# Performance work log

Hardware: AMD Instinct MI355X
Metric: run time of the kernel (lower is better)

## Reference

```python
import jax, jax.numpy as jnp
import numpy as np

STRIDE = 2

def setup_inputs() -> dict:
    key = jax.random.key(0)
    k1, k2, k3, k4, k5 = jax.random.split(key, 5)
    B, Cin, H, W = 16, 64, 128, 128
    Cout, kh, kw = 64, 3, 3
    oh = ow = 63  # ceil((H - kh + 1) / STRIDE)
    inp = jax.random.normal(k1, (B, Cin, H, W), dtype=jnp.float32)
    fan_in = Cin * kh * kw
    weight = jax.random.normal(k2, (Cout, Cin, kh, kw), dtype=jnp.float32) / np.sqrt(fan_in)
    bias = jax.random.normal(k3, (Cout,), dtype=jnp.float32) * 0.01
    selh = jax.random.randint(k4, (oh, ow), 0, STRIDE, dtype=jnp.int32)
    selw = jax.random.randint(k5, (oh, ow), 0, STRIDE, dtype=jnp.int32)
    return {"input": inp, "weight": weight, "bias": bias, "selh": selh, "selw": selw}


def reference(input, weight, bias, selh, selw):
    # Stochastic downsampled conv: per output pixel (i,j), pick the patch at
    # row i*stride + selh[i,j], col j*stride + selw[i,j], then apply the conv GEMM.
    Cout, Cin, kh, kw = weight.shape
    oh, ow = selh.shape
    # top-left corner of the selected patch for each output pixel
    rng_h = selh + jnp.arange(0, oh * STRIDE, STRIDE, dtype=jnp.int32)[:, None]   # (oh, ow)
    rng_w = selw + jnp.arange(0, ow * STRIDE, STRIDE, dtype=jnp.int32)[None, :]   # (oh, ow)
    # full patch index grids: (oh, ow, kh, kw)
    ih = rng_h[:, :, None, None] + jnp.arange(kh, dtype=jnp.int32)[None, None, :, None]
    iw = rng_w[:, :, None, None] + jnp.arange(kw, dtype=jnp.int32)[None, None, None, :]
    # gather selected im2col patches only (avoids materializing the full unfold)
    patches = input[:, :, ih, iw]  # (B, Cin, oh, ow, kh, kw)
    out = jnp.einsum('bcyxhw,ochw->boyx', patches, weight) + bias[None, :, None, None]
    return out  # (B, Cout, oh, ow)
```

## Files before the change

### kernel.cpp

```cpp
#include <hip/hip_runtime.h>


#define B_    16
#define CIN   64
#define H_    128
#define W_    128
#define COUT  64
#define OH    63
#define OW    63
#define NPIX  (OH * OW)
#define KTOT  (CIN * 9)

typedef short  short8  __attribute__((ext_vector_type(8)));
typedef float  float4v __attribute__((ext_vector_type(4)));

__device__ inline short f2bf(float f) {
    union { float f; unsigned u; } x; x.f = f;
    unsigned r = x.u + 0x7fffu + ((x.u >> 16) & 1u);
    return (short)(r >> 16);
}

__global__ __launch_bounds__(256)
void repack_bf16(const float* __restrict__ in, const float* __restrict__ wgt,
                 short* __restrict__ nhwc, short* __restrict__ wgt_t) {
    if (blockIdx.y == H_) {
        const int bid = blockIdx.z * 2 + blockIdx.x;
        for (int e = bid * 256 + (int)threadIdx.x; e < COUT * KTOT; e += 32 * 256) {
            const int o   = e / KTOT;
            const int rem = e - o * KTOT;
            const int c   = rem / 9;
            const int tap = rem - c * 9;
            wgt_t[o * KTOT + tap * CIN + c] = f2bf(wgt[e]);
        }
        return;
    }

    __shared__ float T[64 * 65];
    const int tid = threadIdx.x;
    const int w0  = blockIdx.x * 64;
    const int h   = blockIdx.y;
    const int b   = blockIdx.z;

    {
        const int w4 = tid & 15;
        const int cl = tid >> 4;
#pragma unroll
        for (int i = 0; i < 4; ++i) {
            const int c = cl + 16 * i;
            const float4 v = *(const float4*)&in[((b * CIN + c) * H_ + h) * W_ + w0 + 4 * w4];
            T[c * 65 + 4 * w4 + 0] = v.x;
            T[c * 65 + 4 * w4 + 1] = v.y;
            T[c * 65 + 4 * w4 + 2] = v.z;
            T[c * 65 + 4 * w4 + 3] = v.w;
        }
    }
    __syncthreads();
    {
        const int cg = tid & 7;
        const int wl = tid >> 3;
#pragma unroll
        for (int i = 0; i < 2; ++i) {
            const int w = wl + 32 * i;
            short8 v;
#pragma unroll
            for (int t = 0; t < 8; ++t)
                v[t] = f2bf(T[(8 * cg + t) * 65 + w]);
            *(short8*)&nhwc[((b * H_ + h) * W_ + w0 + w) * CIN + 8 * cg] = v;
        }
    }
}

#define PIXT  16
#define BT    2
#define LDO   65

__global__ __launch_bounds__(256, 4)
void sconv2davg_mfma(const short* __restrict__ nhwc,
                     const short* __restrict__ wgt_t,
                     const float* __restrict__ bias,
                     const int* __restrict__ selh,
                     const int* __restrict__ selw,
                     float* __restrict__ out) {
    __shared__ __align__(16) short As[18 * 1024];

    const int tid = threadIdx.x;
    const int p0  = blockIdx.x * PIXT;
    const int b0  = blockIdx.y * BT;

    const int ln = tid & 15;
    const int hl = (tid >> 4) & 3;
    const int wv = tid >> 6;
    const int l  = tid & 63;

    const short* Bp = &wgt_t[(16 * wv + ln) * KTOT + hl * 8];
    short8 Bv[18];
#pragma unroll
    for (int u = 0; u < 18; ++u) {
        const int cc = u / 9, tap = u - 9 * (u / 9);
        Bv[u] = *(const short8*)&Bp[tap * CIN + cc * 32];
    }

    {
        const int w01 = wv & 1;
        const int wcc = wv >> 1;
        const int mst = 16 * w01 + (l >> 2);
        const int pl  = mst >> 1;
        const int bl  = mst & 1;
        int p = p0 + pl;
        if (p > NPIX - 1) p = NPIX - 1;
        const int y   = p / OW;
        const int x   = p - y * OW;
        const int ih0 = 2 * y + selh[p];
        const int iw0 = 2 * x + selw[p];
        const short* src0 =
            &nhwc[(((b0 + bl) * H_ + ih0) * W_ + iw0) * CIN + wcc * 32 + (l & 3) * 8];
        short* dst0 = &As[wcc * 9 * 1024 + w01 * 512] + l * 8;
#pragma unroll
        for (int tap = 0; tap < 9; ++tap) {
            const int kh = tap / 3, kw = tap - 3 * (tap / 3);
            __builtin_amdgcn_global_load_lds(
                (const __attribute__((address_space(1))) void*)
                    (src0 + kh * (W_ * CIN) + kw * CIN),
                (__attribute__((address_space(3))) void*)(dst0 + tap * 1024),
                16, 0, 0);
        }
    }
    __syncthreads();

    float4v acc[2];
#pragma unroll
    for (int i = 0; i < 2; ++i) acc[i] = (float4v){0.f, 0.f, 0.f, 0.f};
#pragma unroll
    for (int u = 0; u < 18; ++u) {
#pragma unroll
        for (int i = 0; i < 2; ++i) {
            const short8 a = *(const short8*)
                &As[u * 1024 + (16 * i + ln) * 32 + hl * 8];
            acc[i] = __builtin_amdgcn_mfma_f32_16x16x32_bf16(a, Bv[u], acc[i], 0, 0, 0);
        }
    }
    __syncthreads();

    float* Ot = (float*)As;
    const float bv = bias[16 * wv + ln];
#pragma unroll
    for (int i = 0; i < 2; ++i)
#pragma unroll
        for (int r = 0; r < 4; ++r)
            Ot[(16 * i + 4 * hl + r) * LDO + 16 * wv + ln] = acc[i][r] + bv;
    __syncthreads();
    {
        const int pp = tid & 15;
        const int rr = tid >> 4;
        const int p2 = p0 + pp;
        if (p2 < NPIX) {
#pragma unroll
            for (int k = 0; k < 8; ++k) {
                const int rid = k * 16 + rr;
                const int b2  = rid >> 6;
                const int o   = rid & 63;
                out[((b0 + b2) * COUT + o) * NPIX + p2] = Ot[(pp * 2 + b2) * LDO + o];
            }
        }
    }
}

#define FKC   72
#define FLDA  76
__global__ __launch_bounds__(256, 4)
void sconv2davg_fallback(const float* __restrict__ in,
                         const float* __restrict__ wgt,
                         const float* __restrict__ bias,
                         const int* __restrict__ selh,
                         const int* __restrict__ selw,
                         float* __restrict__ out) {
    __shared__ float As[64 * FLDA];
    __shared__ float Ws[64 * FLDA];
    __shared__ int hb_s[4], wb_s[4];
    const int tid = threadIdx.x;
    const int p0  = blockIdx.x * 4;
    if (tid < 4) {
        int p = p0 + tid;
        if (p > NPIX - 1) p = NPIX - 1;
        int y = p / OW;
        int x = p - y * OW;
        hb_s[tid] = 2 * y + selh[p];
        wb_s[tid] = 2 * x + selw[p];
    }
    __syncthreads();
    const int tn = tid & 15, tm = tid >> 4;
    float acc[4][4];
#pragma unroll
    for (int i = 0; i < 4; ++i)
#pragma unroll
        for (int j = 0; j < 4; ++j) acc[i][j] = 0.0f;
    for (int cc = 0; cc < 8; ++cc) {
        const int c0 = cc * 8;
#pragma unroll
        for (int it = 0; it < 18; ++it) {
            int idx = tid + it * 256;
            int m = idx / FKC, rem = idx - m * FKC;
            int cl = rem / 9, r = rem - cl * 9;
            int kh = r / 3, kw = r - kh * 3;
            As[m * FLDA + rem] =
                in[((((m & 15) * CIN) + (c0 + cl)) * H_ + hb_s[m >> 4] + kh) * W_ + wb_s[m >> 4] + kw];
        }
#pragma unroll
        for (int it = 0; it < 18; ++it) {
            int idx = tid + it * 256;
            int o = idx / FKC, kk = idx - o * FKC;
            Ws[o * FLDA + kk] = wgt[o * KTOT + cc * FKC + kk];
        }
        __syncthreads();
#pragma unroll 2
        for (int k0 = 0; k0 < FKC; k0 += 4) {
            float4 a[4], w[4];
#pragma unroll
            for (int i = 0; i < 4; ++i) a[i] = *(const float4*)&As[(4 * tm + i) * FLDA + k0];
#pragma unroll
            for (int j = 0; j < 4; ++j) w[j] = *(const float4*)&Ws[(tn + 16 * j) * FLDA + k0];
#pragma unroll
            for (int i = 0; i < 4; ++i)
#pragma unroll
                for (int j = 0; j < 4; ++j) {
                    acc[i][j] += a[i].x * w[j].x; acc[i][j] += a[i].y * w[j].y;
                    acc[i][j] += a[i].z * w[j].z; acc[i][j] += a[i].w * w[j].w;
                }
        }
        __syncthreads();
    }
    const int p = p0 + (tm >> 2);
    if (p < NPIX) {
#pragma unroll
        for (int i = 0; i < 4; ++i) {
            int b = (tm & 3) * 4 + i;
#pragma unroll
            for (int j = 0; j < 4; ++j)
                out[((b * COUT) + tn + 16 * j) * NPIX + p] = acc[i][j] + bias[tn + 16 * j];
        }
    }
}

extern "C" void kernel_launch(void* const* d_in, const int* in_sizes, int n_in,
                              void* d_out, int out_size, void* d_ws, size_t ws_size,
                              hipStream_t stream) {
    const float* in   = (const float*)d_in[0];
    const float* wgt  = (const float*)d_in[1];
    const float* bias = (const float*)d_in[2];
    const int*   selh = (const int*)d_in[3];
    const int*   selw = (const int*)d_in[4];
    float* out = (float*)d_out;

    const size_t nhwc_elems = (size_t)B_ * H_ * W_ * CIN;
    const size_t need = (nhwc_elems + (size_t)COUT * KTOT) * 2;

    if (ws_size >= need) {
        short* nhwc  = (short*)d_ws;
        short* wgt_t = nhwc + nhwc_elems;
        repack_bf16<<<dim3(W_ / 64, H_ + 1, B_), 256, 0, stream>>>(in, wgt, nhwc, wgt_t);
        const int ptiles = (NPIX + PIXT - 1) / PIXT;
        sconv2davg_mfma<<<dim3(ptiles, B_ / BT), 256, 0, stream>>>(
            nhwc, wgt_t, bias, selh, selw, out);
    } else {
        sconv2davg_fallback<<<(NPIX + 3) / 4, 256, 0, stream>>>(
            in, wgt, bias, selh, selw, out);
    }
}
```

Measured before the change: 129.7 us.

## Process four pixel tiles per block with double-buffered LDS gather prefetch

Each MFMA conv block now handles four consecutive 16-pixel tiles instead of one. It keeps the weight fragments in registers across all four tiles and prefetches the next tile's im2col patches into a second LDS buffer with global_load_lds while the current tile computes. The aim is to amortize per-block weight loading and to overlap gather latency with MFMA work. In exchange, LDS use doubles, the launch-bounds occupancy hint drops from 4 to 2 blocks, and the grid becomes about a quarter the size, which may leave CUs less evenly loaded.

```diff
diff --git a/kernel.cpp b/kernel.cpp
--- a/kernel.cpp
+++ b/kernel.cpp
@@ -72,19 +72,21 @@
 
 #define PIXT  16
 #define BT    2
+#define NT    4
+#define TILE_SH (18 * 1024)
 #define LDO   65
 
-__global__ __launch_bounds__(256, 4)
+__global__ __launch_bounds__(256, 2)
 void sconv2davg_mfma(const short* __restrict__ nhwc,
                      const short* __restrict__ wgt_t,
                      const float* __restrict__ bias,
                      const int* __restrict__ selh,
                      const int* __restrict__ selw,
                      float* __restrict__ out) {
-    __shared__ __align__(16) short As[18 * 1024];
+    __shared__ __align__(16) short As[2 * TILE_SH];
 
     const int tid = threadIdx.x;
-    const int p0  = blockIdx.x * PIXT;
+    const int p00 = blockIdx.x * (PIXT * NT);
     const int b0  = blockIdx.y * BT;
 
     const int ln = tid & 15;
@@ -100,69 +102,89 @@
         Bv[u] = *(const short8*)&Bp[tap * CIN + cc * 32];
     }
 
-    {
-        const int w01 = wv & 1;
-        const int wcc = wv >> 1;
-        const int mst = 16 * w01 + (l >> 2);
-        const int pl  = mst >> 1;
-        const int bl  = mst & 1;
-        int p = p0 + pl;
+    const int w01 = wv & 1;
+    const int wcc = wv >> 1;
+    const int mst = 16 * w01 + (l >> 2);
+    const int pl  = mst >> 1;
+    const int bl  = mst & 1;
+
+    int ih0v[NT], iw0v[NT];
+#pragma unroll
+    for (int t = 0; t < NT; ++t) {
+        int p = p00 + t * PIXT + pl;
         if (p > NPIX - 1) p = NPIX - 1;
-        const int y   = p / OW;
-        const int x   = p - y * OW;
-        const int ih0 = 2 * y + selh[p];
-        const int iw0 = 2 * x + selw[p];
-        const short* src0 =
-            &nhwc[(((b0 + bl) * H_ + ih0) * W_ + iw0) * CIN + wcc * 32 + (l & 3) * 8];
-        short* dst0 = &As[wcc * 9 * 1024 + w01 * 512] + l * 8;
-#pragma unroll
-        for (int tap = 0; tap < 9; ++tap) {
-            const int kh = tap / 3, kw = tap - 3 * (tap / 3);
-            __builtin_amdgcn_global_load_lds(
-                (const __attribute__((address_space(1))) void*)
-                    (src0 + kh * (W_ * CIN) + kw * CIN),
-                (__attribute__((address_space(3))) void*)(dst0 + tap * 1024),
-                16, 0, 0);
-        }
-    }
+        const int y = p / OW;
+        const int x = p - y * OW;
+        ih0v[t] = 2 * y + selh[p];
+        iw0v[t] = 2 * x + selw[p];
+    }
+
+    const short* abase = &nhwc[((size_t)(b0 + bl) * H_) * W_ * CIN + wcc * 32 + (l & 3) * 8];
+    short* dstw = &As[wcc * (9 * 1024) + w01 * 512] + l * 8;
+
+#define STAGE(t, bsel)                                                          \
+    {                                                                           \
+        const short* src0 = abase + (ih0v[t] * W_ + iw0v[t]) * CIN;             \
+        short* dst0 = dstw + (bsel) * TILE_SH;                                  \
+        _Pragma("unroll")                                                       \
+        for (int tap = 0; tap < 9; ++tap) {                                     \
+            const int kh = tap / 3, kw = tap - 3 * (tap / 3);                   \
+            __builtin_amdgcn_global_load_lds(                                   \
+                (const __attribute__((address_space(1))) void*)                 \
+                    (src0 + kh * (W_ * CIN) + kw * CIN),                        \
+                (__attribute__((address_space(3))) void*)(dst0 + tap * 1024),   \
+                16, 0, 0);                                                      \
+        }                                                                       \
+    }
+
+    STAGE(0, 0);
     __syncthreads();
 
-    float4v acc[2];
-#pragma unroll
-    for (int i = 0; i < 2; ++i) acc[i] = (float4v){0.f, 0.f, 0.f, 0.f};
-#pragma unroll
-    for (int u = 0; u < 18; ++u) {
-#pragma unroll
-        for (int i = 0; i < 2; ++i) {
-            const short8 a = *(const short8*)
-                &As[u * 1024 + (16 * i + ln) * 32 + hl * 8];
-            acc[i] = __builtin_amdgcn_mfma_f32_16x16x32_bf16(a, Bv[u], acc[i], 0, 0, 0);
-        }
-    }
-    __syncthreads();
-
-    float* Ot = (float*)As;
     const float bv = bias[16 * wv + ln];
-#pragma unroll
-    for (int i = 0; i < 2; ++i)
-#pragma unroll
-        for (int r = 0; r < 4; ++r)
-            Ot[(16 * i + 4 * hl + r) * LDO + 16 * wv + ln] = acc[i][r] + bv;
-    __syncthreads();
-    {
-        const int pp = tid & 15;
-        const int rr = tid >> 4;
-        const int p2 = p0 + pp;
-        if (p2 < NPIX) {
-#pragma unroll
-            for (int k = 0; k < 8; ++k) {
-                const int rid = k * 16 + rr;
-                const int b2  = rid >> 6;
-                const int o   = rid & 63;
-                out[((b0 + b2) * COUT + o) * NPIX + p2] = Ot[(pp * 2 + b2) * LDO + o];
+    const int pp = tid & 15;
+    const int rr = tid >> 4;
+
+#pragma unroll
+    for (int t = 0; t < NT; ++t) {
+        const int cur = t & 1;
+        if (t + 1 < NT) STAGE(t + 1, (t + 1) & 1);
+
+        float4v acc[2];
+#pragma unroll
+        for (int i = 0; i < 2; ++i) acc[i] = (float4v){0.f, 0.f, 0.f, 0.f};
+#pragma unroll
+        for (int u = 0; u < 18; ++u) {
+#pragma unroll
+            for (int i = 0; i < 2; ++i) {
+                const short8 a = *(const short8*)
+                    &As[cur * TILE_SH + u * 1024 + (16 * i + ln) * 32 + hl * 8];
+                acc[i] = __builtin_amdgcn_mfma_f32_16x16x32_bf16(a, Bv[u], acc[i], 0, 0, 0);
             }
         }
-    }
+        __syncthreads();
+
+        float* Ot = (float*)&As[cur * TILE_SH];
+#pragma unroll
+        for (int i = 0; i < 2; ++i)
+#pragma unroll
+            for (int r = 0; r < 4; ++r)
+                Ot[(16 * i + 4 * hl + r) * LDO + 16 * wv + ln] = acc[i][r] + bv;
+        __syncthreads();
+        {
+            const int p2 = p00 + t * PIXT + pp;
+            if (p2 < NPIX) {
+#pragma unroll
+                for (int k = 0; k < 8; ++k) {
+                    const int rid = k * 16 + rr;
+                    const int b2  = rid >> 6;
+                    const int o   = rid & 63;
+                    out[((b0 + b2) * COUT + o) * NPIX + p2] = Ot[(pp * 2 + b2) * LDO + o];
+                }
+            }
+        }
+        __syncthreads();
+    }
+#undef STAGE
 }
 
 #define FKC   72
@@ -258,8 +280,8 @@
         short* nhwc  = (short*)d_ws;
         short* wgt_t = nhwc + nhwc_elems;
         repack_bf16<<<dim3(W_ / 64, H_ + 1, B_), 256, 0, stream>>>(in, wgt, nhwc, wgt_t);
-        const int ptiles = (NPIX + PIXT - 1) / PIXT;
-        sconv2davg_mfma<<<dim3(ptiles, B_ / BT), 256, 0, stream>>>(
+        const int pblocks = (NPIX + PIXT * NT - 1) / (PIXT * NT);
+        sconv2davg_mfma<<<dim3(pblocks, B_ / BT), 256, 0, stream>>>(
             nhwc, wgt_t, bias, selh, selw, out);
     } else {
         sconv2davg_fallback<<<(NPIX + 3) / 4, 256, 0, stream>>>(
```

Result: faster. 120.8 us (-6.9%).
